# Optimization experiments

Hardware: AMD Instinct MI355X
Metric: run time of the kernel (lower is better)

The kernel has to match this reference:

```python
import jax, jax.numpy as jnp
import numpy as np

LOG2PI = float(np.log(2.0 * np.pi))
NUM_GROUPS = 32
WEIGHTS_THRESHOLD = 0.01
ACTIVATION_THRESHOLD = 1e-9


def _cdist(a, b):
    # a: (..., N, 3), b: (..., M, 3) -> (..., N, M) euclidean distances
    d2 = (jnp.sum(a * a, -1)[..., :, None]
          + jnp.sum(b * b, -1)[..., None, :]
          - 2.0 * jnp.einsum('...nd,...md->...nm', a, b))
    return jnp.sqrt(jnp.maximum(d2, 0.0))


def setup_inputs() -> dict:
    key = jax.random.key(0)
    ks = jax.random.split(key, 7)
    B, V, O, G = 16, 778, 8192, NUM_GROUPS
    verts = jax.random.normal(ks[0], (B, V, 3), jnp.float32)
    anchor_verts = jax.random.normal(ks[1], (B, G, 3), jnp.float32)
    obj_pts = jax.random.normal(ks[2], (B, O, 3), jnp.float32)
    raw = jax.random.normal(ks[3], (B, G, 12), jnp.float32)
    mean = raw[..., :3]
    M = raw[..., 3:].reshape(B, G, 3, 3)
    cov = jnp.einsum('bgij,bgkj->bgik', M, M) + 1e-2 * jnp.eye(3, dtype=jnp.float32)
    contact_gaussians = jnp.concatenate([mean, cov.reshape(B, G, 9)], axis=-1)
    obj_normals = jax.random.normal(ks[4], (B, O, 6), jnp.float32)
    init_verts = jax.random.normal(ks[5], (V, 3), jnp.float32)
    init_anchors = jax.random.normal(ks[6], (G, 3), jnp.float32)
    return dict(verts=verts, anchor_verts=anchor_verts, obj_pts=obj_pts,
                contact_gaussians=contact_gaussians, obj_normals=obj_normals,
                init_verts=init_verts, init_anchors=init_anchors, K=5)


def reference(verts, anchor_verts, obj_pts, contact_gaussians, obj_normals,
              init_verts, init_anchors, K):
    B, V, _ = verts.shape
    G = NUM_GROUPS
    # __init__: assign each vertex to its closest anchor (partition into 32 groups)
    gid = jnp.argmin(_cdist(init_verts, init_anchors), axis=-1)  # (V,)

    # KNN: K smallest distances vertex -> object points
    neigh = _cdist(verts, obj_pts)                 # (B, V, O)
    knn = -jax.lax.top_k(-neigh, K)[0]             # (B, V, K)

    # Per-group MVN log-prob for every vertex (G=32 small, V=778 small)
    mean = contact_gaussians[:, :, :3] + anchor_verts          # (B, G, 3)
    cov = contact_gaussians[:, :, 3:].reshape(B, G, 3, 3)
    L = jnp.linalg.cholesky(cov)                               # (B, G, 3, 3)
    diff = verts[:, None, :, :] - mean[:, :, None, :]          # (B, G, V, 3)
    y = jax.scipy.linalg.solve_triangular(L[:, :, None], diff[..., None], lower=True)[..., 0]
    maha = jnp.sum(y * y, -1)                                  # (B, G, V)
    half_logdet = jnp.sum(jnp.log(jnp.diagonal(L, axis1=-2, axis2=-1)), -1)  # (B, G)
    logp = -0.5 * (maha + 3.0 * LOG2PI) - half_logdet[:, :, None]
    w_all = jnp.exp(logp)                                      # (B, G, V)
    # pick each vertex's own group's weight
    idx = jnp.broadcast_to(gid[None, None, :], (B, 1, V))
    w = jnp.take_along_axis(w_all, idx, axis=1)[:, 0]          # (B, V)

    # per-group min/max normalization (masked, groups partition the vertices)
    grp_mask = gid[None, :] == jnp.arange(G)[:, None]          # (G, V)
    seg_min = jnp.min(jnp.where(grp_mask[None], w[:, None, :], jnp.inf), -1)   # (B, G)
    seg_max = jnp.max(jnp.where(grp_mask[None], w[:, None, :], -jnp.inf), -1)  # (B, G)
    mn = seg_min[:, gid]
    mx = seg_max[:, gid]
    wn = (w - mn) / (mx - mn)
    wn = jnp.where(wn > WEIGHTS_THRESHOLD, wn, 0.0)

    # group activation: torch.allclose(cg[:, i], 0) over whole batch -> zero weight
    active = jnp.any(jnp.abs(contact_gaussians) > ACTIVATION_THRESHOLD, axis=(0, 2))  # (G,)
    eff = jnp.where(active[gid][None, :], wn, 0.0)             # (B, V)
    distances = knn * eff[..., None]
    d_mean = jnp.mean(distances)

    # penetration regularizer using nearest object normal
    ovd = _cdist(verts, obj_normals[..., :3])                  # (B, V, O)
    nn_idx = jnp.argmin(ovd, -1)                               # (B, V)
    nn = jnp.take_along_axis(obj_normals, nn_idx[..., None], axis=1)  # (B, V, 6)
    roots = nn[..., :3] - 0.002 * nn[..., 3:]
    dp = jnp.einsum('bvi,bvi->bv', nn[..., 3:], verts - roots)
    pen = jnp.mean(jax.nn.relu(-dp))
    return (d_mean, pen)
```

## Files before the change

kernel.cpp:

```cpp
#include <hip/hip_runtime.h>
#include <math.h>

#define BB 16
#define VV 778
#define OO 8192
#define GG 32
#define KNN 5
#define THREE_LOG2PI 5.513631199228036f
#define TSCAN 832

#define MED3 __builtin_amdgcn_fmed3f

__device__ __forceinline__ void insert5_med3(float (&t)[KNN], float s) {
    t[4] = MED3(s, t[3], t[4]);
    t[3] = MED3(s, t[2], t[3]);
    t[2] = MED3(s, t[1], t[2]);
    t[1] = MED3(s, t[0], t[1]);
    t[0] = fminf(t[0], s);
}

__device__ __forceinline__ void merge5_med3(float (&m)[KNN], const float (&b)[KNN]) {
    m[4] = MED3(b[0], m[3], m[4]);
    m[3] = MED3(b[0], m[2], m[3]);
    m[2] = MED3(b[0], m[1], m[2]);
    m[1] = MED3(b[0], m[0], m[1]);
    m[0] = fminf(m[0], b[0]);
    m[4] = MED3(b[1], m[3], m[4]);
    m[3] = MED3(b[1], m[2], m[3]);
    m[2] = MED3(b[1], m[1], m[2]);
    m[1] = fminf(m[1], b[1]);
    m[4] = MED3(b[2], m[3], m[4]);
    m[3] = MED3(b[2], m[2], m[3]);
    m[2] = fminf(m[2], b[2]);
    m[4] = MED3(b[3], m[3], m[4]);
    m[3] = fminf(m[3], b[3]);
    m[4] = fminf(m[4], b[4]);
}

__device__ __forceinline__ unsigned int fkey(float s) {
    unsigned int u = __float_as_uint(s);
    unsigned int m = (u & 0x80000000u) ? 0xFFFFFFFFu : 0x80000000u;
    return u ^ m;
}

template <int LOGP>
__global__ __launch_bounds__(TSCAN) void scan_kernel(
    const float* __restrict__ verts,
    const float* __restrict__ anchor_verts,
    const float* __restrict__ obj_pts,
    const float* __restrict__ contact_gaussians,
    const float* __restrict__ obj_normals,
    const float* __restrict__ init_verts,
    const float* __restrict__ init_anchors,
    int* __restrict__ gid_ws,
    float* __restrict__ active_ws,
    float* __restrict__ segmn,
    float* __restrict__ segmx,
    float* __restrict__ w_ws,
    float* __restrict__ top5,
    unsigned long long* __restrict__ pmin,
    float* __restrict__ out) {
    constexpr int P = 1 << LOGP;
    constexpr int NPTS = OO >> LOGP;
    constexpr int CH = (NPTS < 512) ? NPTS : 512;

    __shared__ float4 tile[CH];
    __shared__ float anc[GG * 4];
    __shared__ float cholb[GG * 10];
    __shared__ unsigned short gidl[VV];
    __shared__ unsigned int smn[GG], smx[GG];

    int tid = threadIdx.x;
    int bid = blockIdx.x;

    if (bid < BB * P) {
        int p = bid & (P - 1);
        int b = bid >> LOGP;

        bool valid = tid < VV;
        int vc = valid ? tid : (VV - 1);
        float X, Y, Z;
        {
            const float* vp = verts + ((size_t)b * VV + vc) * 3;
            X = -2.0f * vp[0];
            Y = -2.0f * vp[1];
            Z = -2.0f * vp[2];
        }

        float t[KNN];
#pragma unroll
        for (int k = 0; k < KNN; ++k) t[k] = INFINITY;

        const float* pb = obj_pts + ((size_t)b * OO + p * NPTS) * 3;
        for (int c0 = 0; c0 < NPTS; c0 += CH) {
            if (c0 != 0) __syncthreads();
            for (int j = tid; j < CH; j += TSCAN) {
                const float* q = pb + (size_t)(c0 + j) * 3;
                float a0 = q[0], a1 = q[1], a2 = q[2];
                tile[j] = make_float4(a0, a1, a2, a0 * a0 + a1 * a1 + a2 * a2);
            }
            __syncthreads();
#pragma unroll 8
            for (int i = 0; i < CH; ++i) {
                float4 q = tile[i];
                float sv = fmaf(X, q.x, fmaf(Y, q.y, fmaf(Z, q.z, q.w)));
                insert5_med3(t, sv);
            }
        }
        if (valid) {
            size_t base = ((size_t)(b * P + p) * KNN) * VV + tid;
#pragma unroll
            for (int k = 0; k < KNN; ++k)
                top5[base + (size_t)k * VV] = t[k];
        }
        return;
    }

    {
        int sub = bid - BB * P;
        int p = sub & (P - 1);
        int b = sub >> LOGP;

        bool wduty = (p == 0);
        bool aduty = (p == 1 && b == 0);
        if (wduty || aduty) {
            if (tid < GG) {
                float x = init_anchors[tid * 3 + 0];
                float y = init_anchors[tid * 3 + 1];
                float z = init_anchors[tid * 3 + 2];
                anc[tid * 4 + 0] = x; anc[tid * 4 + 1] = y;
                anc[tid * 4 + 2] = z; anc[tid * 4 + 3] = x * x + y * y + z * z;
                smn[tid] = 0x7F800000u;
                smx[tid] = 0u;
                if (wduty) {
                    const float* cg2 = contact_gaussians + ((size_t)b * GG + tid) * 12;
                    const float* av = anchor_verts + ((size_t)b * GG + tid) * 3;
                    float c00 = cg2[3];
                    float c10 = cg2[6], c11 = cg2[7];
                    float c20 = cg2[9], c21 = cg2[10], c22 = cg2[11];
                    float L00 = sqrtf(c00);
                    float L10 = c10 / L00;
                    float L20 = c20 / L00;
                    float L11 = sqrtf(c11 - L10 * L10);
                    float L21 = (c21 - L20 * L10) / L11;
                    float L22 = sqrtf(c22 - L20 * L20 - L21 * L21);
                    float* c = cholb + tid * 10;
                    c[0] = L00; c[1] = L10; c[2] = L11;
                    c[3] = L20; c[4] = L21; c[5] = L22;
                    c[6] = logf(L00) + logf(L11) + logf(L22);
                    c[7] = cg2[0] + av[0];
                    c[8] = cg2[1] + av[1];
                    c[9] = cg2[2] + av[2];
                }
            }
            __syncthreads();
            for (int v = tid; v < VV; v += TSCAN) {
                float x = init_verts[v * 3 + 0];
                float y = init_verts[v * 3 + 1];
                float z = init_verts[v * 3 + 2];
                float vv = x * x + y * y + z * z;
                float best = INFINITY;
                int bg = 0;
                for (int g = 0; g < GG; ++g) {
                    float d2 = vv + anc[g * 4 + 3] -
                               2.0f * (x * anc[g * 4 + 0] + y * anc[g * 4 + 1] + z * anc[g * 4 + 2]);
                    d2 = fmaxf(d2, 0.0f);
                    if (d2 < best) { best = d2; bg = g; }
                }
                gidl[v] = (unsigned short)bg;
                if (aduty) gid_ws[v] = bg;
            }
            __syncthreads();
            if (wduty) {
                for (int v = tid; v < VV; v += TSCAN) {
                    int g = gidl[v];
                    const float* c = cholb + g * 10;
                    const float* vp = verts + ((size_t)b * VV + v) * 3;
                    float d0 = vp[0] - c[7];
                    float d1 = vp[1] - c[8];
                    float d2 = vp[2] - c[9];
                    float y0 = d0 / c[0];
                    float y1 = (d1 - c[1] * y0) / c[2];
                    float y2 = (d2 - c[3] * y0 - c[4] * y1) / c[5];
                    float maha = y0 * y0 + y1 * y1 + y2 * y2;
                    float wv = expf(-0.5f * (maha + THREE_LOG2PI) - c[6]);
                    w_ws[(size_t)b * VV + v] = wv;
                    unsigned int u = __float_as_uint(wv);
                    atomicMin(&smn[g], u);
                    atomicMax(&smx[g], u);
                }
                __syncthreads();
                if (tid < GG) {
                    segmn[b * GG + tid] = __uint_as_float(smn[tid]);
                    segmx[b * GG + tid] = __uint_as_float(smx[tid]);
                }
            }
            if (aduty) {
                if (tid < GG) {
                    int any = 0;
                    for (int bb = 0; bb < BB && !any; ++bb) {
                        for (int c = 0; c < 12; ++c) {
                            if (fabsf(contact_gaussians[((size_t)bb * GG + tid) * 12 + c]) > 1e-9f) {
                                any = 1;
                                break;
                            }
                        }
                    }
                    active_ws[tid] = any ? 1.0f : 0.0f;
                }
                if (tid == 0) { out[0] = 0.0f; out[1] = 0.0f; }
            }
            __syncthreads();
        }

        bool valid = tid < VV;
        int vc = valid ? tid : (VV - 1);
        float X, Y, Z;
        {
            const float* vp = verts + ((size_t)b * VV + vc) * 3;
            X = -2.0f * vp[0];
            Y = -2.0f * vp[1];
            Z = -2.0f * vp[2];
        }

        float bsv = INFINITY;
        int biv = 0;

        const float* nbp = obj_normals + ((size_t)b * OO + p * NPTS) * 6;
        for (int c0 = 0; c0 < NPTS; c0 += CH) {
            if (c0 != 0) __syncthreads();
            for (int j = tid; j < CH; j += TSCAN) {
                const float* r = nbp + (size_t)(c0 + j) * 6;
                float b0 = r[0], b1 = r[1], b2 = r[2];
                tile[j] = make_float4(b0, b1, b2, b0 * b0 + b1 * b1 + b2 * b2);
            }
            __syncthreads();
#pragma unroll 8
            for (int i = 0; i < CH; ++i) {
                float4 n = tile[i];
                float u = fmaf(X, n.x, fmaf(Y, n.y, fmaf(Z, n.z, n.w)));
                if (u < bsv) { bsv = u; biv = c0 + i; }
            }
        }
        if (valid) {
            unsigned long long key =
                ((unsigned long long)fkey(bsv) << 32) |
                (unsigned int)(p * NPTS + biv);
            pmin[(size_t)(b * P + p) * VV + tid] = key;
        }
    }
}

template <int LOGP>
__global__ __launch_bounds__(256) void finalize_kernel(
    const float* __restrict__ top5,
    const unsigned long long* __restrict__ pmin,
    const float* __restrict__ obj_normals,
    const float* __restrict__ verts,
    const int* __restrict__ gid,
    const float* __restrict__ w,
    const float* __restrict__ segmn,
    const float* __restrict__ segmx,
    const float* __restrict__ active,
    float* __restrict__ out) {
    constexpr int P = 1 << LOGP;
    constexpr int NM = (P + 3) / 4;
    constexpr int NCH = (VV + 63) / 64;

    __shared__ float mt[4][KNN][64];
    __shared__ unsigned long long at[4][64];
    __shared__ float rd[256], rp[256];

    int tid = threadIdx.x;
    int pi = tid >> 6;
    int vi = tid & 63;
    int b = blockIdx.x / NCH;
    int chunk = blockIdx.x - b * NCH;
    int v = chunk * 64 + vi;
    bool valid = v < VV;

    float m[KNN];
#pragma unroll
    for (int k = 0; k < KNN; ++k) m[k] = INFINITY;
    unsigned long long amin = 0xFFFFFFFFFFFFFFFFull;
    if (valid) {
#pragma unroll
        for (int r = 0; r < NM; ++r) {
            int p = pi * NM + r;
            if (p < P) {
                size_t base = ((size_t)(b * P + p) * KNN) * VV + v;
                float t[KNN];
#pragma unroll
                for (int k = 0; k < KNN; ++k) t[k] = top5[base + (size_t)k * VV];
                merge5_med3(m, t);
                unsigned long long a = pmin[(size_t)(b * P + p) * VV + v];
                if (a < amin) amin = a;
            }
        }
    }

#pragma unroll
    for (int k = 0; k < KNN; ++k) mt[pi][k][vi] = m[k];
    at[pi][vi] = amin;
    __syncthreads();

    if (pi < 2) {
        float t[KNN];
#pragma unroll
        for (int k = 0; k < KNN; ++k) t[k] = mt[pi + 2][k][vi];
        merge5_med3(m, t);
#pragma unroll
        for (int k = 0; k < KNN; ++k) mt[pi][k][vi] = m[k];
        unsigned long long a = at[pi + 2][vi];
        if (a < amin) amin = a;
        at[pi][vi] = amin;
    }
    __syncthreads();

    float cd = 0.0f, cp = 0.0f;
    if (pi == 0 && valid) {
        float t[KNN];
#pragma unroll
        for (int k = 0; k < KNN; ++k) t[k] = mt[1][k][vi];
        merge5_med3(m, t);
        unsigned long long a = at[1][vi];
        if (a < amin) amin = a;

        const float* vp = verts + ((size_t)b * VV + v) * 3;
        float vx = vp[0], vy = vp[1], vz = vp[2];
        float vv = vx * vx + vy * vy + vz * vz;

        int g = gid[v];
        float wv = w[(size_t)b * VV + v];
        float mn = segmn[b * GG + g];
        float mx = segmx[b * GG + g];
        float wn = (wv - mn) / (mx - mn);
        float eff = (active[g] != 0.0f && wn > 0.01f) ? wn : 0.0f;
        float sk = 0.0f;
#pragma unroll
        for (int k = 0; k < KNN; ++k) sk += sqrtf(fmaxf(vv + m[k], 0.0f));
        cd = eff * sk;

        int bi = (int)(unsigned int)(amin & 0xFFFFFFFFull);
        const float* row = obj_normals + ((size_t)b * OO + bi) * 6;
        float n0 = row[3], n1 = row[4], n2 = row[5];
        float r0 = row[0] - 0.002f * n0;
        float r1 = row[1] - 0.002f * n1;
        float r2 = row[2] - 0.002f * n2;
        float dp = n0 * (vx - r0) + n1 * (vy - r1) + n2 * (vz - r2);
        cp = fmaxf(-dp, 0.0f);
    }

    rd[tid] = cd;
    rp[tid] = cp;
    __syncthreads();
    for (int s = 128; s > 0; s >>= 1) {
        if (tid < s) {
            rd[tid] += rd[tid + s];
            rp[tid] += rp[tid + s];
        }
        __syncthreads();
    }
    if (tid == 0) {
        atomicAdd(&out[0], rd[0] * (1.0f / ((float)BB * VV * KNN)));
        atomicAdd(&out[1], rp[0] * (1.0f / ((float)BB * VV)));
    }
}

template <int LOGP>
static void launch_all(const float* verts, const float* anchor_verts,
                       const float* obj_pts, const float* contact_gaussians,
                       const float* obj_normals, const float* init_verts,
                       const float* init_anchors, int* gid_ws, float* active_ws,
                       float* segmn, float* segmx, float* w_ws, float* top5,
                       unsigned long long* pmin, float* out, hipStream_t stream) {
    constexpr int P = 1 << LOGP;
    constexpr int NCH = (VV + 63) / 64;
    hipLaunchKernelGGL((scan_kernel<LOGP>), dim3(BB * 2 * P), dim3(TSCAN),
                       0, stream, verts, anchor_verts, obj_pts, contact_gaussians,
                       obj_normals, init_verts, init_anchors, gid_ws, active_ws,
                       segmn, segmx, w_ws, top5, pmin, out);
    hipLaunchKernelGGL((finalize_kernel<LOGP>), dim3(BB * NCH), dim3(256), 0, stream,
                       top5, pmin, obj_normals, verts, gid_ws, w_ws, segmn,
                       segmx, active_ws, out);
}

extern "C" void kernel_launch(void* const* d_in, const int* in_sizes, int n_in,
                              void* d_out, int out_size, void* d_ws, size_t ws_size,
                              hipStream_t stream) {
    const float* verts = (const float*)d_in[0];
    const float* anchor_verts = (const float*)d_in[1];
    const float* obj_pts = (const float*)d_in[2];
    const float* contact_gaussians = (const float*)d_in[3];
    const float* obj_normals = (const float*)d_in[4];
    const float* init_verts = (const float*)d_in[5];
    const float* init_anchors = (const float*)d_in[6];
    float* out = (float*)d_out;

    char* ws = (char*)d_ws;
    int* gid_ws = (int*)(ws + 0);
    float* active_ws = (float*)(ws + 4096);
    float* segmn = (float*)(ws + 4224);
    float* segmx = (float*)(ws + 6272);
    float* w_ws = (float*)(ws + 8320);
    const size_t base = 58368;

    int logP = 4;
    while (logP > 0) {
        size_t need = base + (size_t)BB * (1 << logP) * VV * (KNN * 4 + 8);
        if (need <= ws_size) break;
        --logP;
    }

    unsigned long long* pmin = (unsigned long long*)(ws + base);
    float* top5 = (float*)(ws + base + (size_t)BB * ((size_t)1 << logP) * VV * 8);

#define LAUNCH(L)                                                              \
    launch_all<L>(verts, anchor_verts, obj_pts, contact_gaussians,             \
                  obj_normals, init_verts, init_anchors, gid_ws, active_ws,    \
                  segmn, segmx, w_ws, top5, pmin, out, stream)
    switch (logP) {
        case 4: LAUNCH(4); break;
        case 3: LAUNCH(3); break;
        case 2: LAUNCH(2); break;
        case 1: LAUNCH(1); break;
        default: LAUNCH(0); break;
    }
#undef LAUNCH
}
```

Measured before the change: 123.6 us.

## Stream object points via scalar loads instead of LDS tiles in scan loops

Drops the shared-memory tiling and barriers in both the KNN scan and the nearest-normal scan. Each wavefront now reads object points directly through inline-asm s_load_dwordx4 scalar loads, which are uniform across the block, and computes full squared distances (dx²+dy²+dz²) instead of the expanded dot-product form. The finalize kernel no longer adds the vertex norm. This removes the LDS staging and syncthreads, but it puts an lgkmcnt(0) wait on every iteration, which serializes scalar memory latency. The distance arithmetic also rises from 3 to 6 FLOPs per point.

```diff
diff --git a/kernel.cpp b/kernel.cpp
--- a/kernel.cpp
+++ b/kernel.cpp
@@ -10,6 +10,8 @@
 #define TSCAN 832
 
 #define MED3 __builtin_amdgcn_fmed3f
+
+typedef int i4v __attribute__((ext_vector_type(4)));
 
 __device__ __forceinline__ void insert5_med3(float (&t)[KNN], float s) {
     t[4] = MED3(s, t[3], t[4]);
@@ -41,6 +43,13 @@
     unsigned int u = __float_as_uint(s);
     unsigned int m = (u & 0x80000000u) ? 0xFFFFFFFFu : 0x80000000u;
     return u ^ m;
+}
+
+__device__ __forceinline__ void dist_insert(float (&t)[KNN], float px, float py,
+                                            float pz, float vx, float vy, float vz) {
+    float dx = px - vx, dy = py - vy, dz = pz - vz;
+    float d2 = fmaf(dx, dx, fmaf(dy, dy, dz * dz));
+    insert5_med3(t, d2);
 }
 
 template <int LOGP>
@@ -62,9 +71,7 @@
     float* __restrict__ out) {
     constexpr int P = 1 << LOGP;
     constexpr int NPTS = OO >> LOGP;
-    constexpr int CH = (NPTS < 512) ? NPTS : 512;
-
-    __shared__ float4 tile[CH];
+
     __shared__ float anc[GG * 4];
     __shared__ float cholb[GG * 10];
     __shared__ unsigned short gidl[VV];
@@ -79,33 +86,37 @@
 
         bool valid = tid < VV;
         int vc = valid ? tid : (VV - 1);
-        float X, Y, Z;
+        float vx, vy, vz;
         {
             const float* vp = verts + ((size_t)b * VV + vc) * 3;
-            X = -2.0f * vp[0];
-            Y = -2.0f * vp[1];
-            Z = -2.0f * vp[2];
+            vx = vp[0]; vy = vp[1]; vz = vp[2];
         }
 
         float t[KNN];
 #pragma unroll
         for (int k = 0; k < KNN; ++k) t[k] = INFINITY;
 
-        const float* pb = obj_pts + ((size_t)b * OO + p * NPTS) * 3;
-        for (int c0 = 0; c0 < NPTS; c0 += CH) {
-            if (c0 != 0) __syncthreads();
-            for (int j = tid; j < CH; j += TSCAN) {
-                const float* q = pb + (size_t)(c0 + j) * 3;
-                float a0 = q[0], a1 = q[1], a2 = q[2];
-                tile[j] = make_float4(a0, a1, a2, a0 * a0 + a1 * a1 + a2 * a2);
-            }
-            __syncthreads();
-#pragma unroll 8
-            for (int i = 0; i < CH; ++i) {
-                float4 q = tile[i];
-                float sv = fmaf(X, q.x, fmaf(Y, q.y, fmaf(Z, q.z, q.w)));
-                insert5_med3(t, sv);
-            }
+        unsigned long long addr =
+            (unsigned long long)(obj_pts + ((size_t)b * OO + (size_t)p * NPTS) * 3);
+#pragma unroll 2
+        for (int i = 0; i < NPTS; i += 4) {
+            i4v qa, qb, qc;
+            asm volatile(
+                "s_load_dwordx4 %0, %3, 0x0\n"
+                "s_load_dwordx4 %1, %3, 0x10\n"
+                "s_load_dwordx4 %2, %3, 0x20\n"
+                "s_waitcnt lgkmcnt(0)\n"
+                : "=&s"(qa), "=&s"(qb), "=&s"(qc)
+                : "s"(addr));
+            dist_insert(t, __int_as_float(qa.x), __int_as_float(qa.y),
+                        __int_as_float(qa.z), vx, vy, vz);
+            dist_insert(t, __int_as_float(qa.w), __int_as_float(qb.x),
+                        __int_as_float(qb.y), vx, vy, vz);
+            dist_insert(t, __int_as_float(qb.z), __int_as_float(qb.w),
+                        __int_as_float(qc.x), vx, vy, vz);
+            dist_insert(t, __int_as_float(qc.y), __int_as_float(qc.z),
+                        __int_as_float(qc.w), vx, vy, vz);
+            addr += 48;
         }
         if (valid) {
             size_t base = ((size_t)(b * P + p) * KNN) * VV + tid;
@@ -215,32 +226,42 @@
 
         bool valid = tid < VV;
         int vc = valid ? tid : (VV - 1);
-        float X, Y, Z;
+        float vx, vy, vz;
         {
             const float* vp = verts + ((size_t)b * VV + vc) * 3;
-            X = -2.0f * vp[0];
-            Y = -2.0f * vp[1];
-            Z = -2.0f * vp[2];
+            vx = vp[0]; vy = vp[1]; vz = vp[2];
         }
 
         float bsv = INFINITY;
         int biv = 0;
 
-        const float* nbp = obj_normals + ((size_t)b * OO + p * NPTS) * 6;
-        for (int c0 = 0; c0 < NPTS; c0 += CH) {
-            if (c0 != 0) __syncthreads();
-            for (int j = tid; j < CH; j += TSCAN) {
-                const float* r = nbp + (size_t)(c0 + j) * 6;
-                float b0 = r[0], b1 = r[1], b2 = r[2];
-                tile[j] = make_float4(b0, b1, b2, b0 * b0 + b1 * b1 + b2 * b2);
-            }
-            __syncthreads();
-#pragma unroll 8
-            for (int i = 0; i < CH; ++i) {
-                float4 n = tile[i];
-                float u = fmaf(X, n.x, fmaf(Y, n.y, fmaf(Z, n.z, n.w)));
-                if (u < bsv) { bsv = u; biv = c0 + i; }
-            }
+        unsigned long long addr =
+            (unsigned long long)(obj_normals + ((size_t)b * OO + (size_t)p * NPTS) * 6);
+#pragma unroll 2
+        for (int i = 0; i < NPTS; i += 2) {
+            i4v ra, rb, rc;
+            asm volatile(
+                "s_load_dwordx4 %0, %3, 0x0\n"
+                "s_load_dwordx4 %1, %3, 0x10\n"
+                "s_load_dwordx4 %2, %3, 0x20\n"
+                "s_waitcnt lgkmcnt(0)\n"
+                : "=&s"(ra), "=&s"(rb), "=&s"(rc)
+                : "s"(addr));
+            {
+                float dx = __int_as_float(ra.x) - vx;
+                float dy = __int_as_float(ra.y) - vy;
+                float dz = __int_as_float(ra.z) - vz;
+                float u = fmaf(dx, dx, fmaf(dy, dy, dz * dz));
+                if (u < bsv) { bsv = u; biv = i; }
+            }
+            {
+                float dx = __int_as_float(rb.z) - vx;
+                float dy = __int_as_float(rb.w) - vy;
+                float dz = __int_as_float(rc.x) - vz;
+                float u = fmaf(dx, dx, fmaf(dy, dy, dz * dz));
+                if (u < bsv) { bsv = u; biv = i + 1; }
+            }
+            addr += 48;
         }
         if (valid) {
             unsigned long long key =
@@ -328,7 +349,6 @@
 
         const float* vp = verts + ((size_t)b * VV + v) * 3;
         float vx = vp[0], vy = vp[1], vz = vp[2];
-        float vv = vx * vx + vy * vy + vz * vz;
 
         int g = gid[v];
         float wv = w[(size_t)b * VV + v];
@@ -338,7 +358,7 @@
         float eff = (active[g] != 0.0f && wn > 0.01f) ? wn : 0.0f;
         float sk = 0.0f;
 #pragma unroll
-        for (int k = 0; k < KNN; ++k) sk += sqrtf(fmaxf(vv + m[k], 0.0f));
+        for (int k = 0; k < KNN; ++k) sk += sqrtf(fmaxf(m[k], 0.0f));
         cd = eff * sk;
 
         int bi = (int)(unsigned int)(amin & 0xFFFFFFFFull);
```

Measured after the change: 190.8 us. +54.4%, slower.

## Split weight/gid setup into separate blocks and stagger tile scan start offsets

Applied to the files above, without the earlier changes.

Moves the per-batch Gaussian weight computation and the group-id/activation setup out of the normal-scan blocks into BB+1 dedicated extra blocks, so scan blocks no longer carry serial prologue work that delays them. Each wave starts its shared-memory tile sweep at a different offset (by wave and block parity) to spread LDS bank access. The nearest-normal search now uses exact squared differences packed into a 64-bit key with a single compare instead of the dot-product form with a separate index. This adds more blocks, and the sign-bit OR on the key relies on the finalize kernel's key decoding being consistent.

```diff
diff --git a/kernel.cpp b/kernel.cpp
--- a/kernel.cpp
+++ b/kernel.cpp
@@ -72,6 +72,7 @@
 
     int tid = threadIdx.x;
     int bid = blockIdx.x;
+    int woff = ((((tid >> 6) << 1) | (bid & 1)) * 20) & (CH - 1);
 
     if (bid < BB * P) {
         int p = bid & (P - 1);
@@ -101,11 +102,17 @@
             }
             __syncthreads();
 #pragma unroll 8
-            for (int i = 0; i < CH; ++i) {
+            for (int i = woff; i < CH; ++i) {
                 float4 q = tile[i];
                 float sv = fmaf(X, q.x, fmaf(Y, q.y, fmaf(Z, q.z, q.w)));
                 insert5_med3(t, sv);
             }
+#pragma unroll 8
+            for (int i = 0; i < woff; ++i) {
+                float4 q = tile[i];
+                float sv = fmaf(X, q.x, fmaf(Y, q.y, fmaf(Z, q.z, q.w)));
+                insert5_med3(t, sv);
+            }
         }
         if (valid) {
             size_t base = ((size_t)(b * P + p) * KNN) * VV + tid;
@@ -116,14 +123,64 @@
         return;
     }
 
-    {
+    if (bid < 2 * BB * P) {
         int sub = bid - BB * P;
         int p = sub & (P - 1);
         int b = sub >> LOGP;
 
-        bool wduty = (p == 0);
-        bool aduty = (p == 1 && b == 0);
-        if (wduty || aduty) {
+        bool valid = tid < VV;
+        int vc = valid ? tid : (VV - 1);
+        float vx, vy, vz;
+        {
+            const float* vp = verts + ((size_t)b * VV + vc) * 3;
+            vx = vp[0]; vy = vp[1]; vz = vp[2];
+        }
+
+        unsigned long long kmin = 0xFFFFFFFFFFFFFFFFull;
+
+        const float* nbp = obj_normals + ((size_t)b * OO + p * NPTS) * 6;
+        for (int c0 = 0; c0 < NPTS; c0 += CH) {
+            if (c0 != 0) __syncthreads();
+            for (int j = tid; j < CH; j += TSCAN) {
+                const float* r = nbp + (size_t)(c0 + j) * 6;
+                float b0 = r[0], b1 = r[1], b2 = r[2];
+                tile[j] = make_float4(b0, b1, b2, 0.0f);
+            }
+            __syncthreads();
+#pragma unroll 8
+            for (int i = woff; i < CH; ++i) {
+                float4 q = tile[i];
+                float dx = q.x - vx, dy = q.y - vy, dz = q.z - vz;
+                float u = fmaf(dx, dx, fmaf(dy, dy, dz * dz));
+                unsigned long long key =
+                    ((unsigned long long)__float_as_uint(u) << 32) |
+                    (unsigned int)(c0 + i);
+                if (key < kmin) kmin = key;
+            }
+#pragma unroll 8
+            for (int i = 0; i < woff; ++i) {
+                float4 q = tile[i];
+                float dx = q.x - vx, dy = q.y - vy, dz = q.z - vz;
+                float u = fmaf(dx, dx, fmaf(dy, dy, dz * dz));
+                unsigned long long key =
+                    ((unsigned long long)__float_as_uint(u) << 32) |
+                    (unsigned int)(c0 + i);
+                if (key < kmin) kmin = key;
+            }
+        }
+        if (valid) {
+            unsigned int ub = (unsigned int)(kmin >> 32);
+            unsigned int gi = (unsigned int)kmin + (unsigned int)(p * NPTS);
+            pmin[(size_t)(b * P + p) * VV + tid] =
+                ((unsigned long long)(ub | 0x80000000u) << 32) | gi;
+        }
+        return;
+    }
+
+    {
+        int d = bid - 2 * BB * P;
+        if (d < BB) {
+            int b = d;
             if (tid < GG) {
                 float x = init_anchors[tid * 3 + 0];
                 float y = init_anchors[tid * 3 + 1];
@@ -132,26 +189,24 @@
                 anc[tid * 4 + 2] = z; anc[tid * 4 + 3] = x * x + y * y + z * z;
                 smn[tid] = 0x7F800000u;
                 smx[tid] = 0u;
-                if (wduty) {
-                    const float* cg2 = contact_gaussians + ((size_t)b * GG + tid) * 12;
-                    const float* av = anchor_verts + ((size_t)b * GG + tid) * 3;
-                    float c00 = cg2[3];
-                    float c10 = cg2[6], c11 = cg2[7];
-                    float c20 = cg2[9], c21 = cg2[10], c22 = cg2[11];
-                    float L00 = sqrtf(c00);
-                    float L10 = c10 / L00;
-                    float L20 = c20 / L00;
-                    float L11 = sqrtf(c11 - L10 * L10);
-                    float L21 = (c21 - L20 * L10) / L11;
-                    float L22 = sqrtf(c22 - L20 * L20 - L21 * L21);
-                    float* c = cholb + tid * 10;
-                    c[0] = L00; c[1] = L10; c[2] = L11;
-                    c[3] = L20; c[4] = L21; c[5] = L22;
-                    c[6] = logf(L00) + logf(L11) + logf(L22);
-                    c[7] = cg2[0] + av[0];
-                    c[8] = cg2[1] + av[1];
-                    c[9] = cg2[2] + av[2];
-                }
+                const float* cg2 = contact_gaussians + ((size_t)b * GG + tid) * 12;
+                const float* av = anchor_verts + ((size_t)b * GG + tid) * 3;
+                float c00 = cg2[3];
+                float c10 = cg2[6], c11 = cg2[7];
+                float c20 = cg2[9], c21 = cg2[10], c22 = cg2[11];
+                float L00 = sqrtf(c00);
+                float L10 = c10 / L00;
+                float L20 = c20 / L00;
+                float L11 = sqrtf(c11 - L10 * L10);
+                float L21 = (c21 - L20 * L10) / L11;
+                float L22 = sqrtf(c22 - L20 * L20 - L21 * L21);
+                float* c = cholb + tid * 10;
+                c[0] = L00; c[1] = L10; c[2] = L11;
+                c[3] = L20; c[4] = L21; c[5] = L22;
+                c[6] = logf(L00) + logf(L11) + logf(L22);
+                c[7] = cg2[0] + av[0];
+                c[8] = cg2[1] + av[1];
+                c[9] = cg2[2] + av[2];
             }
             __syncthreads();
             for (int v = tid; v < VV; v += TSCAN) {
@@ -168,85 +223,67 @@
                     if (d2 < best) { best = d2; bg = g; }
                 }
                 gidl[v] = (unsigned short)bg;
-                if (aduty) gid_ws[v] = bg;
-            }
-            __syncthreads();
-            if (wduty) {
-                for (int v = tid; v < VV; v += TSCAN) {
-                    int g = gidl[v];
-                    const float* c = cholb + g * 10;
-                    const float* vp = verts + ((size_t)b * VV + v) * 3;
-                    float d0 = vp[0] - c[7];
-                    float d1 = vp[1] - c[8];
-                    float d2 = vp[2] - c[9];
-                    float y0 = d0 / c[0];
-                    float y1 = (d1 - c[1] * y0) / c[2];
-                    float y2 = (d2 - c[3] * y0 - c[4] * y1) / c[5];
-                    float maha = y0 * y0 + y1 * y1 + y2 * y2;
-                    float wv = expf(-0.5f * (maha + THREE_LOG2PI) - c[6]);
-                    w_ws[(size_t)b * VV + v] = wv;
-                    unsigned int u = __float_as_uint(wv);
-                    atomicMin(&smn[g], u);
-                    atomicMax(&smx[g], u);
+            }
+            __syncthreads();
+            for (int v = tid; v < VV; v += TSCAN) {
+                int g = gidl[v];
+                const float* c = cholb + g * 10;
+                const float* vp = verts + ((size_t)b * VV + v) * 3;
+                float d0 = vp[0] - c[7];
+                float d1 = vp[1] - c[8];
+                float d2 = vp[2] - c[9];
+                float y0 = d0 / c[0];
+                float y1 = (d1 - c[1] * y0) / c[2];
+                float y2 = (d2 - c[3] * y0 - c[4] * y1) / c[5];
+                float maha = y0 * y0 + y1 * y1 + y2 * y2;
+                float wv = expf(-0.5f * (maha + THREE_LOG2PI) - c[6]);
+                w_ws[(size_t)b * VV + v] = wv;
+                unsigned int u = __float_as_uint(wv);
+                atomicMin(&smn[g], u);
+                atomicMax(&smx[g], u);
+            }
+            __syncthreads();
+            if (tid < GG) {
+                segmn[b * GG + tid] = __uint_as_float(smn[tid]);
+                segmx[b * GG + tid] = __uint_as_float(smx[tid]);
+            }
+        } else {
+            if (tid < GG) {
+                float x = init_anchors[tid * 3 + 0];
+                float y = init_anchors[tid * 3 + 1];
+                float z = init_anchors[tid * 3 + 2];
+                anc[tid * 4 + 0] = x; anc[tid * 4 + 1] = y;
+                anc[tid * 4 + 2] = z; anc[tid * 4 + 3] = x * x + y * y + z * z;
+            }
+            __syncthreads();
+            for (int v = tid; v < VV; v += TSCAN) {
+                float x = init_verts[v * 3 + 0];
+                float y = init_verts[v * 3 + 1];
+                float z = init_verts[v * 3 + 2];
+                float vv = x * x + y * y + z * z;
+                float best = INFINITY;
+                int bg = 0;
+                for (int g = 0; g < GG; ++g) {
+                    float d2 = vv + anc[g * 4 + 3] -
+                               2.0f * (x * anc[g * 4 + 0] + y * anc[g * 4 + 1] + z * anc[g * 4 + 2]);
+                    d2 = fmaxf(d2, 0.0f);
+                    if (d2 < best) { best = d2; bg = g; }
                 }
-                __syncthreads();
-                if (tid < GG) {
-                    segmn[b * GG + tid] = __uint_as_float(smn[tid]);
-                    segmx[b * GG + tid] = __uint_as_float(smx[tid]);
-                }
-            }
-            if (aduty) {
-                if (tid < GG) {
-                    int any = 0;
-                    for (int bb = 0; bb < BB && !any; ++bb) {
-                        for (int c = 0; c < 12; ++c) {
-                            if (fabsf(contact_gaussians[((size_t)bb * GG + tid) * 12 + c]) > 1e-9f) {
-                                any = 1;
-                                break;
-                            }
+                gid_ws[v] = bg;
+            }
+            if (tid < GG) {
+                int any = 0;
+                for (int bb = 0; bb < BB && !any; ++bb) {
+                    for (int c = 0; c < 12; ++c) {
+                        if (fabsf(contact_gaussians[((size_t)bb * GG + tid) * 12 + c]) > 1e-9f) {
+                            any = 1;
+                            break;
                         }
                     }
-                    active_ws[tid] = any ? 1.0f : 0.0f;
                 }
-                if (tid == 0) { out[0] = 0.0f; out[1] = 0.0f; }
-            }
-            __syncthreads();
-        }
-
-        bool valid = tid < VV;
-        int vc = valid ? tid : (VV - 1);
-        float X, Y, Z;
-        {
-            const float* vp = verts + ((size_t)b * VV + vc) * 3;
-            X = -2.0f * vp[0];
-            Y = -2.0f * vp[1];
-            Z = -2.0f * vp[2];
-        }
-
-        float bsv = INFINITY;
-        int biv = 0;
-
-        const float* nbp = obj_normals + ((size_t)b * OO + p * NPTS) * 6;
-        for (int c0 = 0; c0 < NPTS; c0 += CH) {
-            if (c0 != 0) __syncthreads();
-            for (int j = tid; j < CH; j += TSCAN) {
-                const float* r = nbp + (size_t)(c0 + j) * 6;
-                float b0 = r[0], b1 = r[1], b2 = r[2];
-                tile[j] = make_float4(b0, b1, b2, b0 * b0 + b1 * b1 + b2 * b2);
-            }
-            __syncthreads();
-#pragma unroll 8
-            for (int i = 0; i < CH; ++i) {
-                float4 n = tile[i];
-                float u = fmaf(X, n.x, fmaf(Y, n.y, fmaf(Z, n.z, n.w)));
-                if (u < bsv) { bsv = u; biv = c0 + i; }
-            }
-        }
-        if (valid) {
-            unsigned long long key =
-                ((unsigned long long)fkey(bsv) << 32) |
-                (unsigned int)(p * NPTS + biv);
-            pmin[(size_t)(b * P + p) * VV + tid] = key;
+                active_ws[tid] = any ? 1.0f : 0.0f;
+            }
+            if (tid == 0) { out[0] = 0.0f; out[1] = 0.0f; }
         }
     }
 }
@@ -376,7 +413,7 @@
                        unsigned long long* pmin, float* out, hipStream_t stream) {
     constexpr int P = 1 << LOGP;
     constexpr int NCH = (VV + 63) / 64;
-    hipLaunchKernelGGL((scan_kernel<LOGP>), dim3(BB * 2 * P), dim3(TSCAN),
+    hipLaunchKernelGGL((scan_kernel<LOGP>), dim3(BB * 2 * P + BB + 1), dim3(TSCAN),
                        0, stream, verts, anchor_verts, obj_pts, contact_gaussians,
                        obj_normals, init_verts, init_anchors, gid_ws, active_ws,
                        segmn, segmx, w_ws, top5, pmin, out);
```

After: 132.4 us. +7.2%, slower.

## Store packed xyz tiles in LDS and compute direct squared differences

Applied to the files above, without the earlier changes.

Object points are now copied into shared memory as packed xyz triples using float4 vector loads, in place of padded float4 tiles that carried a precomputed squared norm. Distances are computed as direct squared differences, so the vertex norm no longer has to be added back in the finalize step. The normals scan uses the same packed layout and processes four points per iteration. This cuts LDS footprint and global load instructions, but adds a few more ALU ops per point (subtractions instead of the dot-product form).

```diff
diff --git a/kernel.cpp b/kernel.cpp
--- a/kernel.cpp
+++ b/kernel.cpp
@@ -64,7 +64,7 @@
     constexpr int NPTS = OO >> LOGP;
     constexpr int CH = (NPTS < 512) ? NPTS : 512;
 
-    __shared__ float4 tile[CH];
+    __shared__ float4 tp[(CH * 3) / 4];
     __shared__ float anc[GG * 4];
     __shared__ float cholb[GG * 10];
     __shared__ unsigned short gidl[VV];
@@ -79,32 +79,43 @@
 
         bool valid = tid < VV;
         int vc = valid ? tid : (VV - 1);
-        float X, Y, Z;
+        float vx, vy, vz;
         {
             const float* vp = verts + ((size_t)b * VV + vc) * 3;
-            X = -2.0f * vp[0];
-            Y = -2.0f * vp[1];
-            Z = -2.0f * vp[2];
+            vx = vp[0]; vy = vp[1]; vz = vp[2];
         }
 
         float t[KNN];
 #pragma unroll
         for (int k = 0; k < KNN; ++k) t[k] = INFINITY;
 
-        const float* pb = obj_pts + ((size_t)b * OO + p * NPTS) * 3;
+        const float* pb = obj_pts + ((size_t)b * OO + (size_t)p * NPTS) * 3;
         for (int c0 = 0; c0 < NPTS; c0 += CH) {
             if (c0 != 0) __syncthreads();
-            for (int j = tid; j < CH; j += TSCAN) {
-                const float* q = pb + (size_t)(c0 + j) * 3;
-                float a0 = q[0], a1 = q[1], a2 = q[2];
-                tile[j] = make_float4(a0, a1, a2, a0 * a0 + a1 * a1 + a2 * a2);
-            }
+            const float4* gp = (const float4*)(pb + (size_t)c0 * 3);
+            for (int j = tid; j < (CH * 3) / 4; j += TSCAN) tp[j] = gp[j];
             __syncthreads();
-#pragma unroll 8
-            for (int i = 0; i < CH; ++i) {
-                float4 q = tile[i];
-                float sv = fmaf(X, q.x, fmaf(Y, q.y, fmaf(Z, q.z, q.w)));
-                insert5_med3(t, sv);
+#pragma unroll 4
+            for (int j = 0; j < CH / 4; ++j) {
+                float4 A = tp[3 * j + 0];
+                float4 B = tp[3 * j + 1];
+                float4 C = tp[3 * j + 2];
+                {
+                    float dx = A.x - vx, dy = A.y - vy, dz = A.z - vz;
+                    insert5_med3(t, fmaf(dx, dx, fmaf(dy, dy, dz * dz)));
+                }
+                {
+                    float dx = A.w - vx, dy = B.x - vy, dz = B.y - vz;
+                    insert5_med3(t, fmaf(dx, dx, fmaf(dy, dy, dz * dz)));
+                }
+                {
+                    float dx = B.z - vx, dy = B.w - vy, dz = C.x - vz;
+                    insert5_med3(t, fmaf(dx, dx, fmaf(dy, dy, dz * dz)));
+                }
+                {
+                    float dx = C.y - vx, dy = C.z - vy, dz = C.w - vz;
+                    insert5_med3(t, fmaf(dx, dx, fmaf(dy, dy, dz * dz)));
+                }
             }
         }
         if (valid) {
@@ -215,31 +226,52 @@
 
         bool valid = tid < VV;
         int vc = valid ? tid : (VV - 1);
-        float X, Y, Z;
+        float vx, vy, vz;
         {
             const float* vp = verts + ((size_t)b * VV + vc) * 3;
-            X = -2.0f * vp[0];
-            Y = -2.0f * vp[1];
-            Z = -2.0f * vp[2];
+            vx = vp[0]; vy = vp[1]; vz = vp[2];
         }
 
         float bsv = INFINITY;
         int biv = 0;
 
-        const float* nbp = obj_normals + ((size_t)b * OO + p * NPTS) * 6;
+        const float* nbp = obj_normals + ((size_t)b * OO + (size_t)p * NPTS) * 6;
+        float* t3 = (float*)tp;
         for (int c0 = 0; c0 < NPTS; c0 += CH) {
             if (c0 != 0) __syncthreads();
             for (int j = tid; j < CH; j += TSCAN) {
                 const float* r = nbp + (size_t)(c0 + j) * 6;
-                float b0 = r[0], b1 = r[1], b2 = r[2];
-                tile[j] = make_float4(b0, b1, b2, b0 * b0 + b1 * b1 + b2 * b2);
+                t3[3 * j + 0] = r[0];
+                t3[3 * j + 1] = r[1];
+                t3[3 * j + 2] = r[2];
             }
             __syncthreads();
-#pragma unroll 8
-            for (int i = 0; i < CH; ++i) {
-                float4 n = tile[i];
-                float u = fmaf(X, n.x, fmaf(Y, n.y, fmaf(Z, n.z, n.w)));
-                if (u < bsv) { bsv = u; biv = c0 + i; }
+#pragma unroll 4
+            for (int j = 0; j < CH / 4; ++j) {
+                float4 A = tp[3 * j + 0];
+                float4 B = tp[3 * j + 1];
+                float4 C = tp[3 * j + 2];
+                int gi = c0 + 4 * j;
+                {
+                    float dx = A.x - vx, dy = A.y - vy, dz = A.z - vz;
+                    float u = fmaf(dx, dx, fmaf(dy, dy, dz * dz));
+                    if (u < bsv) { bsv = u; biv = gi; }
+                }
+                {
+                    float dx = A.w - vx, dy = B.x - vy, dz = B.y - vz;
+                    float u = fmaf(dx, dx, fmaf(dy, dy, dz * dz));
+                    if (u < bsv) { bsv = u; biv = gi + 1; }
+                }
+                {
+                    float dx = B.z - vx, dy = B.w - vy, dz = C.x - vz;
+                    float u = fmaf(dx, dx, fmaf(dy, dy, dz * dz));
+                    if (u < bsv) { bsv = u; biv = gi + 2; }
+                }
+                {
+                    float dx = C.y - vx, dy = C.z - vy, dz = C.w - vz;
+                    float u = fmaf(dx, dx, fmaf(dy, dy, dz * dz));
+                    if (u < bsv) { bsv = u; biv = gi + 3; }
+                }
             }
         }
         if (valid) {
@@ -328,7 +360,6 @@
 
         const float* vp = verts + ((size_t)b * VV + v) * 3;
         float vx = vp[0], vy = vp[1], vz = vp[2];
-        float vv = vx * vx + vy * vy + vz * vz;
 
         int g = gid[v];
         float wv = w[(size_t)b * VV + v];
@@ -338,7 +369,7 @@
         float eff = (active[g] != 0.0f && wn > 0.01f) ? wn : 0.0f;
         float sk = 0.0f;
 #pragma unroll
-        for (int k = 0; k < KNN; ++k) sk += sqrtf(fmaxf(vv + m[k], 0.0f));
+        for (int k = 0; k < KNN; ++k) sk += sqrtf(fmaxf(m[k], 0.0f));
         cd = eff * sk;
 
         int bi = (int)(unsigned int)(amin & 0xFFFFFFFFull);
```

After: 130.9 us. 1.06x slower.
